# Performance work log

Hardware: AMD Instinct MI355X
Metric: run time of the kernel (lower is better)

Reference implementation:

```python
import jax, jax.numpy as jnp
import numpy as np

B, L, C, H = 4, 2048, 1024, 16
D = C // H  # head_dim = 64


def setup_inputs() -> dict:
    key = jax.random.key(0)
    ks = jax.random.split(key, 7)
    x = jax.random.normal(ks[0], (B, L, C), dtype=jnp.float32)
    Wqkv = jax.random.normal(ks[1], (C, 3 * C), dtype=jnp.float32) * 0.02
    bqkv = jnp.zeros((3 * C,), dtype=jnp.float32)
    q_gamma = jnp.ones((H, D), dtype=jnp.float32)
    k_gamma = jnp.ones((H, D), dtype=jnp.float32)
    Wout = jax.random.normal(ks[2], (C, C), dtype=jnp.float32) * 0.02
    bout = jnp.zeros((C,), dtype=jnp.float32)
    return {"x": x, "Wqkv": Wqkv, "bqkv": bqkv, "q_gamma": q_gamma,
            "k_gamma": k_gamma, "Wout": Wout, "bout": bout}


def _mh_rms_norm(t, gamma):
    # F.normalize(x.float(), dim=-1) * gamma * sqrt(dim), cast back to input dtype
    tf = t.astype(jnp.float32)
    n = jnp.sqrt(jnp.sum(tf * tf, axis=-1, keepdims=True))
    normed = tf / jnp.maximum(n, 1e-12)
    return (normed * gamma * jnp.sqrt(jnp.float32(t.shape[-1]))).astype(t.dtype)


def reference(x, Wqkv, bqkv, q_gamma, k_gamma, Wout, bout):
    b, l, c = x.shape
    qkv = (x @ Wqkv + bqkv).reshape(b, l, 3, H, D)
    q, k, v = qkv[:, :, 0], qkv[:, :, 1], qkv[:, :, 2]  # [B, L, H, D]
    q = _mh_rms_norm(q, q_gamma)
    k = _mh_rms_norm(k, k_gamma)
    # scaled dot-product attention in BLHD layout
    scale = 1.0 / jnp.sqrt(jnp.float32(D))
    scores = jnp.einsum('blhd,bmhd->bhlm', q, k) * scale  # [B, H, L, L]
    probs = jax.nn.softmax(scores, axis=-1)
    h = jnp.einsum('bhlm,bmhd->blhd', probs, v)  # [B, L, H, D]
    h = h.reshape(b, l, c)
    return h @ Wout + bout
```

## Files before the change

kernel.cpp:

```cpp
#include <hip/hip_runtime.h>
#include <hip/hip_bf16.h>
#include <cstdint>
#include <cstddef>

#define B_ 4
#define L_ 2048
#define C_ 1024
#define H_ 16
#define D_ 64

typedef __bf16    bf16x2 __attribute__((ext_vector_type(2)));
typedef __bf16    bf16x4 __attribute__((ext_vector_type(4)));
typedef __bf16    bf16x8 __attribute__((ext_vector_type(8)));
typedef _Float16  f16x4  __attribute__((ext_vector_type(4)));
typedef _Float16  f16x8  __attribute__((ext_vector_type(8)));
typedef float     f32x4  __attribute__((ext_vector_type(4)));

typedef const __attribute__((address_space(1))) uint32_t* gas_ptr;
typedef __attribute__((address_space(3))) uint32_t* las_ptr;
__device__ __forceinline__ void gl_lds16(const void* g, void* l) {
    __builtin_amdgcn_global_load_lds((gas_ptr)(uintptr_t)g,
                                     (las_ptr)(uintptr_t)l, 16, 0, 0);
}

__global__ __launch_bounds__(256) void prep_kernel(
    const float* __restrict__ x, _Float16* __restrict__ x16,
    const float* __restrict__ Wqkv, _Float16* __restrict__ Wq16,
    const float* __restrict__ Wout, _Float16* __restrict__ Wo16)
{
    __shared__ float tile[64][65];
    int bid = blockIdx.x;
    const int tid = threadIdx.x;

    if (bid < 8192) {
        int i = (bid * 256 + tid) * 4;
        float4 v = *(const float4*)&x[i];
        f16x4 o = {(_Float16)v.x, (_Float16)v.y, (_Float16)v.z, (_Float16)v.w};
        *(f16x4*)&x16[i] = o;
        return;
    }
    bid -= 8192;
    const float* W; _Float16* Wt; int N, tx, ty;
    if (bid < 768) { W = Wqkv; Wt = Wq16; N = 3072; tx = bid % 48; ty = bid / 48; }
    else { bid -= 768; W = Wout; Wt = Wo16; N = 1024; tx = bid % 16; ty = bid / 16; }
    const int K = 1024;
    const int k0 = ty * 64, n0 = tx * 64;
    for (int i = tid; i < 1024; i += 256) {
        int r = i >> 4, c4 = (i & 15) * 4;
        float4 v = *(const float4*)&W[(size_t)(k0 + r) * N + n0 + c4];
        tile[r][c4 + 0] = v.x; tile[r][c4 + 1] = v.y;
        tile[r][c4 + 2] = v.z; tile[r][c4 + 3] = v.w;
    }
    __syncthreads();
    for (int i = tid; i < 1024; i += 256) {
        int n = i >> 4, k4 = (i & 15) * 4;
        f16x4 o = {(_Float16)tile[k4 + 0][n], (_Float16)tile[k4 + 1][n],
                   (_Float16)tile[k4 + 2][n], (_Float16)tile[k4 + 3][n]};
        *(f16x4*)&Wt[(size_t)(n0 + n) * K + k0 + k4] = o;
    }
}

template <int MODE>
__global__ __launch_bounds__(256) void gemm_f16_bt_kernel(
    const _Float16* __restrict__ A, const _Float16* __restrict__ Bt,
    const float* __restrict__ bias, void* __restrict__ Cout,
    __bf16* __restrict__ vTout, const float* __restrict__ q_gamma,
    const float* __restrict__ k_gamma, int M, int N, int K)
{
    __shared__ __align__(16) char smraw[MODE == 1 ? 34816 : 16384];
    _Float16* Ash = (_Float16*)smraw;
    _Float16* Bsh = Ash + 128 * 32;

    const int tid  = threadIdx.x;
    const int lane = tid & 63;
    const int wv   = tid >> 6;
    const int wm   = wv & 1, wn = wv >> 1;
    const int n16  = lane & 15, quad = lane >> 4;
    const int brow = blockIdx.y * 128;
    const int bcol = blockIdx.x * 128;

    const int srow = lane >> 2;
    const int scol = (lane & 3) * 8;
    const _Float16* gA = A  + (size_t)(brow + wv * 32 + srow) * K + scol;
    const _Float16* gB = Bt + (size_t)(bcol + wv * 32 + srow) * K + scol;
    _Float16* lA0 = &Ash[wv * 1024];
    _Float16* lA1 = &Ash[wv * 1024 + 512];
    _Float16* lB0 = &Bsh[wv * 1024];
    _Float16* lB1 = &Bsh[wv * 1024 + 512];

    f32x4 acc[4][4] = {};

    for (int k0 = 0; k0 < K; k0 += 32) {
        gl_lds16(gA + k0,                  lA0);
        gl_lds16(gA + k0 + 16 * (size_t)K, lA1);
        gl_lds16(gB + k0,                  lB0);
        gl_lds16(gB + k0 + 16 * (size_t)K, lB1);
        __syncthreads();

        f16x8 ar[4], br[4];
        #pragma unroll
        for (int t = 0; t < 4; t++) {
            ar[t] = *(const f16x8*)&Ash[(wm * 64 + t * 16 + n16) * 32 + quad * 8];
            br[t] = *(const f16x8*)&Bsh[(wn * 64 + t * 16 + n16) * 32 + quad * 8];
        }
        #pragma unroll
        for (int i = 0; i < 4; i++)
            #pragma unroll
            for (int j = 0; j < 4; j++)
                acc[i][j] = __builtin_amdgcn_mfma_f32_16x16x32_f16(
                    ar[i], br[j], acc[i][j], 0, 0, 0);
        __syncthreads();
    }

    if (MODE == 0) {
        #pragma unroll
        for (int j = 0; j < 4; j++) {
            const int col = bcol + wn * 64 + j * 16 + n16;
            const float bv = bias[col];
            #pragma unroll
            for (int i = 0; i < 4; i++) {
                const int row0 = brow + wm * 64 + i * 16 + quad * 4;
                #pragma unroll
                for (int r = 0; r < 4; r++)
                    ((float*)Cout)[(size_t)(row0 + r) * N + col] = acc[i][j][r] + bv;
            }
        }
        return;
    }

    const int region = bcol >> 10;
    float bj[4];
    #pragma unroll
    for (int j = 0; j < 4; j++) bj[j] = bias[bcol + wn * 64 + j * 16 + n16];

    if (region < 2) {
        const float* gamma = (region == 0) ? q_gamma : k_gamma;
        const float scl = (region == 0) ? 1.44269504f : 8.0f;
        const int cb = (bcol & 1023) + wn * 64 + n16;
        float gj[4];
        #pragma unroll
        for (int j = 0; j < 4; j++) gj[j] = gamma[cb + j * 16];

        #pragma unroll
        for (int i = 0; i < 4; i++) {
            #pragma unroll
            for (int r = 0; r < 4; r++) {
                float v0 = acc[i][0][r] + bj[0];
                float v1 = acc[i][1][r] + bj[1];
                float v2 = acc[i][2][r] + bj[2];
                float v3 = acc[i][3][r] + bj[3];
                float ss = v0 * v0 + v1 * v1 + v2 * v2 + v3 * v3;
                ss += __shfl_xor(ss, 1, 64);
                ss += __shfl_xor(ss, 2, 64);
                ss += __shfl_xor(ss, 4, 64);
                ss += __shfl_xor(ss, 8, 64);
                const float sc = scl / fmaxf(sqrtf(ss), 1e-12f);
                const int row = brow + wm * 64 + i * 16 + quad * 4 + r;
                __bf16* op = (__bf16*)Cout + (size_t)row * 3072 + bcol + wn * 64 + n16;
                op[ 0] = (__bf16)(v0 * gj[0] * sc);
                op[16] = (__bf16)(v1 * gj[1] * sc);
                op[32] = (__bf16)(v2 * gj[2] * sc);
                op[48] = (__bf16)(v3 * gj[3] * sc);
            }
        }
    } else {
        __syncthreads();
        __bf16* LT = (__bf16*)smraw;
        #pragma unroll
        for (int i = 0; i < 4; i++)
            #pragma unroll
            for (int j = 0; j < 4; j++) {
                const int col = wn * 64 + j * 16 + n16;
                const int row0 = wm * 64 + i * 16 + quad * 4;
                bf16x4 t4 = {(__bf16)(acc[i][j][0] + bj[j]),
                             (__bf16)(acc[i][j][1] + bj[j]),
                             (__bf16)(acc[i][j][2] + bj[j]),
                             (__bf16)(acc[i][j][3] + bj[j])};
                *(bf16x4*)&LT[col * 136 + row0] = t4;
            }
        __syncthreads();
        const int d = tid >> 1, hf = tid & 1;
        const int bidx = brow >> 11;
        const int l0 = (brow & 2047) + hf * 64;
        const int head = ((bcol - 2048) >> 6) + (d >> 6);
        const size_t vb = (((size_t)(bidx * 16 + head)) * 64 + (d & 63)) * 2048 + l0;
        #pragma unroll
        for (int u = 0; u < 8; u++)
            *(bf16x8*)&vTout[vb + u * 8] = *(const bf16x8*)&LT[d * 136 + hf * 64 + u * 8];
    }
}

__global__ __launch_bounds__(256) void attn_mfma_kernel(
    const __bf16* __restrict__ qkv, const __bf16* __restrict__ vT,
    _Float16* __restrict__ h16)
{
    const int tid  = threadIdx.x;
    const int lane = tid & 63;
    const int wv   = tid >> 6;
    const int n16  = lane & 15;
    const int quad = lane >> 4;
    const int qt = blockIdx.x & 15;
    const int hh = (blockIdx.x >> 4) & 15;
    const int bb = blockIdx.x >> 8;
    const int q0 = qt * 128;
    const int w32 = wv * 32;
    const int bh = bb * 16 + hh;

    __shared__ __align__(16) __bf16 smem[128 * 72 + 4 * 64 * 64];
    __bf16* QP   = smem;
    __bf16* Kbuf = smem + 128 * 72;
    __bf16* Vbuf = Kbuf + 2 * 64 * 64;

    const __bf16* kbase = &qkv[(size_t)(bb * L_) * 3072 + 1024 + hh * 64];
    const __bf16* vbase = &vT[(size_t)bh * 64 * 2048];

    const int lr = lane >> 3;
    const int lc = (lane & 7) ^ lr;
    const __bf16* kpre = kbase + (size_t)(wv * 8 + lr) * 3072 + lc * 8;
    const __bf16* vpre = vbase + (size_t)(wv * 8 + lr) * 2048 + lc * 8;
    __bf16* kdst = Kbuf + (wv * 8) * 64;
    __bf16* vdst = Vbuf + (wv * 8) * 64;

    #pragma unroll
    for (int t = 0; t < 2; t++) {
        gl_lds16(kpre + (size_t)t * 32 * 3072, kdst + t * 2048);
        gl_lds16(vpre + (size_t)t * 32 * 2048, vdst + t * 2048);
    }

    #pragma unroll
    for (int t = 0; t < 4; t++) {
        int i = tid + t * 256;
        int r = i >> 3, d8 = (i & 7) * 8;
        *(bf16x8*)&QP[r * 72 + d8] =
            *(const bf16x8*)&qkv[(size_t)(bb * L_ + q0 + r) * 3072 + hh * 64 + d8];
    }
    __syncthreads();

    bf16x8 qf[2][2];
    #pragma unroll
    for (int qg = 0; qg < 2; qg++)
        #pragma unroll
        for (int hf = 0; hf < 2; hf++)
            qf[qg][hf] = *(const bf16x8*)&QP[(w32 + qg * 16 + n16) * 72 + hf * 32 + quad * 8];
    __syncthreads();

    f32x4 O[2][4] = {};
    float l_run[2] = {0.f, 0.f};

    const int bk0 = n16 * 64 + ((quad)     ^ (n16 & 7)) * 8;
    const int bk1 = n16 * 64 + ((quad + 4) ^ (n16 & 7)) * 8;

    for (int j0 = 0, cur = 0; j0 < L_; j0 += 64, cur ^= 1) {
        if (j0 + 64 < L_) {
            const __bf16* kp = kpre + (size_t)(j0 + 64) * 3072;
            const __bf16* vp = vpre + (j0 + 64);
            __bf16* kd = kdst + (cur ^ 1) * 4096;
            __bf16* vd = vdst + (cur ^ 1) * 4096;
            #pragma unroll
            for (int t = 0; t < 2; t++) {
                gl_lds16(kp + (size_t)t * 32 * 3072, kd + t * 2048);
                gl_lds16(vp + (size_t)t * 32 * 2048, vd + t * 2048);
            }
        }
        const __bf16* Kc = Kbuf + cur * 4096;
        const __bf16* Vc = Vbuf + cur * 4096;

        f32x4 St[2][4] = {};
        __builtin_amdgcn_s_setprio(1);
        #pragma unroll
        for (int kg = 0; kg < 4; kg++) {
            bf16x8 a0 = *(const bf16x8*)&Kc[kg * 1024 + bk0];
            bf16x8 a1 = *(const bf16x8*)&Kc[kg * 1024 + bk1];
            St[0][kg] = __builtin_amdgcn_mfma_f32_16x16x32_bf16(a0, qf[0][0], St[0][kg], 0, 0, 0);
            St[0][kg] = __builtin_amdgcn_mfma_f32_16x16x32_bf16(a1, qf[0][1], St[0][kg], 0, 0, 0);
            St[1][kg] = __builtin_amdgcn_mfma_f32_16x16x32_bf16(a0, qf[1][0], St[1][kg], 0, 0, 0);
            St[1][kg] = __builtin_amdgcn_mfma_f32_16x16x32_bf16(a1, qf[1][1], St[1][kg], 0, 0, 0);
        }
        __builtin_amdgcn_s_setprio(0);

        #pragma unroll
        for (int qg = 0; qg < 2; qg++) {
            const int prow = (w32 + qg * 16 + n16) * 72;
            float ts = 0.f;
            #pragma unroll
            for (int kg = 0; kg < 4; kg++) {
                float p0 = __builtin_amdgcn_exp2f(St[qg][kg][0]);
                float p1 = __builtin_amdgcn_exp2f(St[qg][kg][1]);
                float p2 = __builtin_amdgcn_exp2f(St[qg][kg][2]);
                float p3 = __builtin_amdgcn_exp2f(St[qg][kg][3]);
                bf16x4 t4 = {(__bf16)p0, (__bf16)p1, (__bf16)p2, (__bf16)p3};
                *(bf16x4*)&QP[prow + kg * 16 + quad * 4] = t4;
                ts += (p0 + p1) + (p2 + p3);
            }
            ts += __shfl_xor(ts, 16, 64);
            ts += __shfl_xor(ts, 32, 64);
            l_run[qg] += ts;
        }

        bf16x8 pf[2][2];
        #pragma unroll
        for (int qg = 0; qg < 2; qg++)
            #pragma unroll
            for (int kh = 0; kh < 2; kh++)
                pf[qg][kh] = *(const bf16x8*)&QP[(w32 + qg * 16 + n16) * 72 + kh * 32 + quad * 8];

        __builtin_amdgcn_s_setprio(1);
        #pragma unroll
        for (int dg = 0; dg < 4; dg++) {
            bf16x8 v0 = *(const bf16x8*)&Vc[dg * 1024 + bk0];
            bf16x8 v1 = *(const bf16x8*)&Vc[dg * 1024 + bk1];
            O[0][dg] = __builtin_amdgcn_mfma_f32_16x16x32_bf16(v0, pf[0][0], O[0][dg], 0, 0, 0);
            O[0][dg] = __builtin_amdgcn_mfma_f32_16x16x32_bf16(v1, pf[0][1], O[0][dg], 0, 0, 0);
            O[1][dg] = __builtin_amdgcn_mfma_f32_16x16x32_bf16(v0, pf[1][0], O[1][dg], 0, 0, 0);
            O[1][dg] = __builtin_amdgcn_mfma_f32_16x16x32_bf16(v1, pf[1][1], O[1][dg], 0, 0, 0);
        }
        __builtin_amdgcn_s_setprio(0);

        __syncthreads();
    }

    #pragma unroll
    for (int qg = 0; qg < 2; qg++) {
        const float linv = 1.0f / l_run[qg];
        const int q = q0 + w32 + qg * 16 + n16;
        const size_t orow = (size_t)(bb * L_ + q) * 1024 + hh * 64 + quad * 4;
        #pragma unroll
        for (int dg = 0; dg < 4; dg++) {
            f16x4 o = {(_Float16)(O[qg][dg][0] * linv),
                       (_Float16)(O[qg][dg][1] * linv),
                       (_Float16)(O[qg][dg][2] * linv),
                       (_Float16)(O[qg][dg][3] * linv)};
            *(f16x4*)&h16[orow + dg * 16] = o;
        }
    }
}

extern "C" void kernel_launch(void* const* d_in, const int* in_sizes, int n_in,
                              void* d_out, int out_size, void* d_ws, size_t ws_size,
                              hipStream_t stream)
{
    const float* x       = (const float*)d_in[0];
    const float* Wqkv    = (const float*)d_in[1];
    const float* bqkv    = (const float*)d_in[2];
    const float* q_gamma = (const float*)d_in[3];
    const float* k_gamma = (const float*)d_in[4];
    const float* Wout    = (const float*)d_in[5];
    const float* bout    = (const float*)d_in[6];
    float* out = (float*)d_out;

    uint8_t* ws = (uint8_t*)d_ws;
    _Float16* x16   = (_Float16*)(ws);
    _Float16* Wq16  = (_Float16*)(ws + (16ull << 20));
    _Float16* Wo16  = (_Float16*)(ws + (22ull << 20));
    __bf16*   qkv16 = (__bf16*)  (ws + (24ull << 20));
    _Float16* h16   = (_Float16*)(ws + (72ull << 20));
    __bf16*   vT    = (__bf16*)  (ws + (88ull << 20));

    prep_kernel<<<8192 + 768 + 256, 256, 0, stream>>>(x, x16, Wqkv, Wq16, Wout, Wo16);

    gemm_f16_bt_kernel<1><<<dim3(3 * C_ / 128, B_ * L_ / 128), 256, 0, stream>>>(
        x16, Wq16, bqkv, qkv16, vT, q_gamma, k_gamma, B_ * L_, 3 * C_, C_);

    attn_mfma_kernel<<<B_ * H_ * (L_ / 128), 256, 0, stream>>>(qkv16, vT, h16);

    gemm_f16_bt_kernel<0><<<dim3(C_ / 128, B_ * L_ / 128), 256, 0, stream>>>(
        h16, Wo16, bout, out, nullptr, nullptr, nullptr, B_ * L_, C_, C_);
}
```

Measured before the change: 306.6 us.

## Load V fragments directly from global and drop V LDS staging

V tiles are no longer staged through double-buffered LDS. Each wave now reads its V MFMA fragments straight from the transposed V buffer in global memory, issued after the QK^T MFMAs so the latency can hide behind the softmax. Q fragments are also read directly from global instead of through LDS, and launch bounds ask for 4 blocks per CU. The LDS cut is meant to raise occupancy, but every wave in a block now fetches the same V data separately, which leans on L1/L2 and exposes global latency inside the loop.

```diff
diff --git a/kernel.cpp b/kernel.cpp
--- a/kernel.cpp
+++ b/kernel.cpp
@@ -190,7 +190,7 @@
     }
 }
 
-__global__ __launch_bounds__(256) void attn_mfma_kernel(
+__global__ __launch_bounds__(256, 4) void attn_mfma_kernel(
     const __bf16* __restrict__ qkv, const __bf16* __restrict__ vT,
     _Float16* __restrict__ h16)
 {
@@ -206,10 +206,9 @@
     const int w32 = wv * 32;
     const int bh = bb * 16 + hh;
 
-    __shared__ __align__(16) __bf16 smem[128 * 72 + 4 * 64 * 64];
+    __shared__ __align__(16) __bf16 smem[128 * 72 + 2 * 64 * 64];
     __bf16* QP   = smem;
     __bf16* Kbuf = smem + 128 * 72;
-    __bf16* Vbuf = Kbuf + 2 * 64 * 64;
 
     const __bf16* kbase = &qkv[(size_t)(bb * L_) * 3072 + 1024 + hh * 64];
     const __bf16* vbase = &vT[(size_t)bh * 64 * 2048];
@@ -217,53 +216,39 @@
     const int lr = lane >> 3;
     const int lc = (lane & 7) ^ lr;
     const __bf16* kpre = kbase + (size_t)(wv * 8 + lr) * 3072 + lc * 8;
-    const __bf16* vpre = vbase + (size_t)(wv * 8 + lr) * 2048 + lc * 8;
     __bf16* kdst = Kbuf + (wv * 8) * 64;
-    __bf16* vdst = Vbuf + (wv * 8) * 64;
 
     #pragma unroll
-    for (int t = 0; t < 2; t++) {
+    for (int t = 0; t < 2; t++)
         gl_lds16(kpre + (size_t)t * 32 * 3072, kdst + t * 2048);
-        gl_lds16(vpre + (size_t)t * 32 * 2048, vdst + t * 2048);
-    }
-
-    #pragma unroll
-    for (int t = 0; t < 4; t++) {
-        int i = tid + t * 256;
-        int r = i >> 3, d8 = (i & 7) * 8;
-        *(bf16x8*)&QP[r * 72 + d8] =
-            *(const bf16x8*)&qkv[(size_t)(bb * L_ + q0 + r) * 3072 + hh * 64 + d8];
-    }
-    __syncthreads();
 
     bf16x8 qf[2][2];
+    const __bf16* qrow = &qkv[(size_t)(bb * L_ + q0 + w32 + n16) * 3072 + hh * 64 + quad * 8];
     #pragma unroll
     for (int qg = 0; qg < 2; qg++)
         #pragma unroll
         for (int hf = 0; hf < 2; hf++)
-            qf[qg][hf] = *(const bf16x8*)&QP[(w32 + qg * 16 + n16) * 72 + hf * 32 + quad * 8];
-    __syncthreads();
+            qf[qg][hf] = *(const bf16x8*)&qrow[(size_t)qg * 16 * 3072 + hf * 32];
+
+    const __bf16* vrow = vbase + (size_t)n16 * 2048 + quad * 8;
 
     f32x4 O[2][4] = {};
     float l_run[2] = {0.f, 0.f};
 
     const int bk0 = n16 * 64 + ((quad)     ^ (n16 & 7)) * 8;
     const int bk1 = n16 * 64 + ((quad + 4) ^ (n16 & 7)) * 8;
+
+    __syncthreads();
 
     for (int j0 = 0, cur = 0; j0 < L_; j0 += 64, cur ^= 1) {
         if (j0 + 64 < L_) {
             const __bf16* kp = kpre + (size_t)(j0 + 64) * 3072;
-            const __bf16* vp = vpre + (j0 + 64);
             __bf16* kd = kdst + (cur ^ 1) * 4096;
-            __bf16* vd = vdst + (cur ^ 1) * 4096;
-            #pragma unroll
-            for (int t = 0; t < 2; t++) {
+            #pragma unroll
+            for (int t = 0; t < 2; t++)
                 gl_lds16(kp + (size_t)t * 32 * 3072, kd + t * 2048);
-                gl_lds16(vp + (size_t)t * 32 * 2048, vd + t * 2048);
-            }
         }
         const __bf16* Kc = Kbuf + cur * 4096;
-        const __bf16* Vc = Vbuf + cur * 4096;
 
         f32x4 St[2][4] = {};
         __builtin_amdgcn_s_setprio(1);
@@ -277,6 +262,13 @@
             St[1][kg] = __builtin_amdgcn_mfma_f32_16x16x32_bf16(a1, qf[1][1], St[1][kg], 0, 0, 0);
         }
         __builtin_amdgcn_s_setprio(0);
+
+        bf16x8 vf[4][2];
+        #pragma unroll
+        for (int dg = 0; dg < 4; dg++)
+            #pragma unroll
+            for (int kh = 0; kh < 2; kh++)
+                vf[dg][kh] = *(const bf16x8*)&vrow[(size_t)dg * 16 * 2048 + j0 + kh * 32];
 
         #pragma unroll
         for (int qg = 0; qg < 2; qg++) {
@@ -307,12 +299,10 @@
         __builtin_amdgcn_s_setprio(1);
         #pragma unroll
         for (int dg = 0; dg < 4; dg++) {
-            bf16x8 v0 = *(const bf16x8*)&Vc[dg * 1024 + bk0];
-            bf16x8 v1 = *(const bf16x8*)&Vc[dg * 1024 + bk1];
-            O[0][dg] = __builtin_amdgcn_mfma_f32_16x16x32_bf16(v0, pf[0][0], O[0][dg], 0, 0, 0);
-            O[0][dg] = __builtin_amdgcn_mfma_f32_16x16x32_bf16(v1, pf[0][1], O[0][dg], 0, 0, 0);
-            O[1][dg] = __builtin_amdgcn_mfma_f32_16x16x32_bf16(v0, pf[1][0], O[1][dg], 0, 0, 0);
-            O[1][dg] = __builtin_amdgcn_mfma_f32_16x16x32_bf16(v1, pf[1][1], O[1][dg], 0, 0, 0);
+            O[0][dg] = __builtin_amdgcn_mfma_f32_16x16x32_bf16(vf[dg][0], pf[0][0], O[0][dg], 0, 0, 0);
+            O[0][dg] = __builtin_amdgcn_mfma_f32_16x16x32_bf16(vf[dg][1], pf[0][1], O[0][dg], 0, 0, 0);
+            O[1][dg] = __builtin_amdgcn_mfma_f32_16x16x32_bf16(vf[dg][0], pf[1][0], O[1][dg], 0, 0, 0);
+            O[1][dg] = __builtin_amdgcn_mfma_f32_16x16x32_bf16(vf[dg][1], pf[1][1], O[1][dg], 0, 0, 0);
         }
         __builtin_amdgcn_s_setprio(0);
 
```

Measured after the change: 365.4 us. 19.2% more time.

## Use 32x32x16 MFMA in attention and keep P in registers via permlane swap

Applied to the files above, without the earlier changes.

Rewrites the attention inner loop to use 32x32x16 bf16 MFMA tiles with 32 query rows per wave. The softmax probabilities now go straight from the S accumulator layout into the B-operand layout of the PV MFMA using v_cvt_pk_bf16_f32 and v_permlane32_swap. This removes the LDS round trip for P and the staging of Q through shared memory. LDS use drops, and launch bounds request 4 blocks per SM for occupancy, at the cost of larger register accumulators and reliance on gfx950-specific instructions and layout correctness.

```diff
diff --git a/kernel.cpp b/kernel.cpp
--- a/kernel.cpp
+++ b/kernel.cpp
@@ -15,12 +15,23 @@
 typedef _Float16  f16x4  __attribute__((ext_vector_type(4)));
 typedef _Float16  f16x8  __attribute__((ext_vector_type(8)));
 typedef float     f32x4  __attribute__((ext_vector_type(4)));
+typedef float     f32x16 __attribute__((ext_vector_type(16)));
+typedef uint32_t  u32x4  __attribute__((ext_vector_type(4)));
 
 typedef const __attribute__((address_space(1))) uint32_t* gas_ptr;
 typedef __attribute__((address_space(3))) uint32_t* las_ptr;
 __device__ __forceinline__ void gl_lds16(const void* g, void* l) {
     __builtin_amdgcn_global_load_lds((gas_ptr)(uintptr_t)g,
                                      (las_ptr)(uintptr_t)l, 16, 0, 0);
+}
+
+__device__ __forceinline__ uint32_t cvtpk_bf16(float lo, float hi) {
+    uint32_t r;
+    asm("v_cvt_pk_bf16_f32 %0, %1, %2" : "=v"(r) : "v"(lo), "v"(hi));
+    return r;
+}
+__device__ __forceinline__ void plswap(uint32_t& a, uint32_t& b) {
+    asm("v_permlane32_swap_b32 %0, %1" : "+v"(a), "+v"(b));
 }
 
 __global__ __launch_bounds__(256) void prep_kernel(
@@ -190,26 +201,25 @@
     }
 }
 
-__global__ __launch_bounds__(256) void attn_mfma_kernel(
+__global__ __launch_bounds__(256, 4) void attn_mfma_kernel(
     const __bf16* __restrict__ qkv, const __bf16* __restrict__ vT,
     _Float16* __restrict__ h16)
 {
     const int tid  = threadIdx.x;
     const int lane = tid & 63;
     const int wv   = tid >> 6;
-    const int n16  = lane & 15;
-    const int quad = lane >> 4;
+    const int l31  = lane & 31;
+    const int h    = lane >> 5;
+    const int x7   = l31 & 7;
     const int qt = blockIdx.x & 15;
     const int hh = (blockIdx.x >> 4) & 15;
     const int bb = blockIdx.x >> 8;
     const int q0 = qt * 128;
-    const int w32 = wv * 32;
     const int bh = bb * 16 + hh;
 
-    __shared__ __align__(16) __bf16 smem[128 * 72 + 4 * 64 * 64];
-    __bf16* QP   = smem;
-    __bf16* Kbuf = smem + 128 * 72;
-    __bf16* Vbuf = Kbuf + 2 * 64 * 64;
+    __shared__ __align__(16) __bf16 smem[4 * 4096];
+    __bf16* Kbuf = smem;
+    __bf16* Vbuf = smem + 2 * 4096;
 
     const __bf16* kbase = &qkv[(size_t)(bb * L_) * 3072 + 1024 + hh * 64];
     const __bf16* vbase = &vT[(size_t)bh * 64 * 2048];
@@ -227,111 +237,97 @@
         gl_lds16(vpre + (size_t)t * 32 * 2048, vdst + t * 2048);
     }
 
+    bf16x8 qf[4];
+    const __bf16* qptr = &qkv[(size_t)(bb * L_ + q0 + wv * 32 + l31) * 3072
+                              + hh * 64 + h * 8];
     #pragma unroll
-    for (int t = 0; t < 4; t++) {
-        int i = tid + t * 256;
-        int r = i >> 3, d8 = (i & 7) * 8;
-        *(bf16x8*)&QP[r * 72 + d8] =
-            *(const bf16x8*)&qkv[(size_t)(bb * L_ + q0 + r) * 3072 + hh * 64 + d8];
-    }
+    for (int dk = 0; dk < 4; dk++)
+        qf[dk] = *(const bf16x8*)&qptr[dk * 16];
+
+    f32x16 acc0 = {}, acc1 = {};
+    float l_run = 0.f;
+
     __syncthreads();
-
-    bf16x8 qf[2][2];
-    #pragma unroll
-    for (int qg = 0; qg < 2; qg++)
-        #pragma unroll
-        for (int hf = 0; hf < 2; hf++)
-            qf[qg][hf] = *(const bf16x8*)&QP[(w32 + qg * 16 + n16) * 72 + hf * 32 + quad * 8];
-    __syncthreads();
-
-    f32x4 O[2][4] = {};
-    float l_run[2] = {0.f, 0.f};
-
-    const int bk0 = n16 * 64 + ((quad)     ^ (n16 & 7)) * 8;
-    const int bk1 = n16 * 64 + ((quad + 4) ^ (n16 & 7)) * 8;
 
     for (int j0 = 0, cur = 0; j0 < L_; j0 += 64, cur ^= 1) {
         if (j0 + 64 < L_) {
-            const __bf16* kp = kpre + (size_t)(j0 + 64) * 3072;
-            const __bf16* vp = vpre + (j0 + 64);
-            __bf16* kd = kdst + (cur ^ 1) * 4096;
-            __bf16* vd = vdst + (cur ^ 1) * 4096;
             #pragma unroll
             for (int t = 0; t < 2; t++) {
-                gl_lds16(kp + (size_t)t * 32 * 3072, kd + t * 2048);
-                gl_lds16(vp + (size_t)t * 32 * 2048, vd + t * 2048);
+                gl_lds16(kpre + (size_t)(j0 + 64 + t * 32) * 3072,
+                         kdst + (cur ^ 1) * 4096 + t * 2048);
+                gl_lds16(vpre + (j0 + 64) + (size_t)t * 32 * 2048,
+                         vdst + (cur ^ 1) * 4096 + t * 2048);
             }
         }
         const __bf16* Kc = Kbuf + cur * 4096;
         const __bf16* Vc = Vbuf + cur * 4096;
 
-        f32x4 St[2][4] = {};
+        f32x16 St0 = {}, St1 = {};
         __builtin_amdgcn_s_setprio(1);
         #pragma unroll
-        for (int kg = 0; kg < 4; kg++) {
-            bf16x8 a0 = *(const bf16x8*)&Kc[kg * 1024 + bk0];
-            bf16x8 a1 = *(const bf16x8*)&Kc[kg * 1024 + bk1];
-            St[0][kg] = __builtin_amdgcn_mfma_f32_16x16x32_bf16(a0, qf[0][0], St[0][kg], 0, 0, 0);
-            St[0][kg] = __builtin_amdgcn_mfma_f32_16x16x32_bf16(a1, qf[0][1], St[0][kg], 0, 0, 0);
-            St[1][kg] = __builtin_amdgcn_mfma_f32_16x16x32_bf16(a0, qf[1][0], St[1][kg], 0, 0, 0);
-            St[1][kg] = __builtin_amdgcn_mfma_f32_16x16x32_bf16(a1, qf[1][1], St[1][kg], 0, 0, 0);
+        for (int dk = 0; dk < 4; dk++) {
+            const int co = ((2 * dk + h) ^ x7) * 8;
+            bf16x8 k0 = *(const bf16x8*)&Kc[l31 * 64 + co];
+            bf16x8 k1 = *(const bf16x8*)&Kc[(32 + l31) * 64 + co];
+            St0 = __builtin_amdgcn_mfma_f32_32x32x16_bf16(k0, qf[dk], St0, 0, 0, 0);
+            St1 = __builtin_amdgcn_mfma_f32_32x32x16_bf16(k1, qf[dk], St1, 0, 0, 0);
         }
         __builtin_amdgcn_s_setprio(0);
 
-        #pragma unroll
-        for (int qg = 0; qg < 2; qg++) {
-            const int prow = (w32 + qg * 16 + n16) * 72;
-            float ts = 0.f;
-            #pragma unroll
-            for (int kg = 0; kg < 4; kg++) {
-                float p0 = __builtin_amdgcn_exp2f(St[qg][kg][0]);
-                float p1 = __builtin_amdgcn_exp2f(St[qg][kg][1]);
-                float p2 = __builtin_amdgcn_exp2f(St[qg][kg][2]);
-                float p3 = __builtin_amdgcn_exp2f(St[qg][kg][3]);
-                bf16x4 t4 = {(__bf16)p0, (__bf16)p1, (__bf16)p2, (__bf16)p3};
-                *(bf16x4*)&QP[prow + kg * 16 + quad * 4] = t4;
-                ts += (p0 + p1) + (p2 + p3);
-            }
-            ts += __shfl_xor(ts, 16, 64);
-            ts += __shfl_xor(ts, 32, 64);
-            l_run[qg] += ts;
-        }
-
-        bf16x8 pf[2][2];
-        #pragma unroll
-        for (int qg = 0; qg < 2; qg++)
-            #pragma unroll
-            for (int kh = 0; kh < 2; kh++)
-                pf[qg][kh] = *(const bf16x8*)&QP[(w32 + qg * 16 + n16) * 72 + kh * 32 + quad * 8];
+        bf16x8 pf[4];
+        float ts = 0.f;
+        #pragma unroll
+        for (int th = 0; th < 2; th++) {
+            float e[16];
+            #pragma unroll
+            for (int r = 0; r < 16; r++) {
+                e[r] = __builtin_amdgcn_exp2f(th == 0 ? St0[r] : St1[r]);
+                ts += e[r];
+            }
+            uint32_t a0 = cvtpk_bf16(e[0], e[1]),  a1 = cvtpk_bf16(e[2], e[3]);
+            uint32_t b0 = cvtpk_bf16(e[4], e[5]),  b1 = cvtpk_bf16(e[6], e[7]);
+            plswap(a0, b0); plswap(a1, b1);
+            u32x4 w0; w0.x = a0; w0.y = a1; w0.z = b0; w0.w = b1;
+            pf[th * 2 + 0] = __builtin_bit_cast(bf16x8, w0);
+            uint32_t c0 = cvtpk_bf16(e[8], e[9]),   c1 = cvtpk_bf16(e[10], e[11]);
+            uint32_t d0 = cvtpk_bf16(e[12], e[13]), d1 = cvtpk_bf16(e[14], e[15]);
+            plswap(c0, d0); plswap(c1, d1);
+            u32x4 w1; w1.x = c0; w1.y = c1; w1.z = d0; w1.w = d1;
+            pf[th * 2 + 1] = __builtin_bit_cast(bf16x8, w1);
+        }
+        l_run += ts;
 
         __builtin_amdgcn_s_setprio(1);
         #pragma unroll
-        for (int dg = 0; dg < 4; dg++) {
-            bf16x8 v0 = *(const bf16x8*)&Vc[dg * 1024 + bk0];
-            bf16x8 v1 = *(const bf16x8*)&Vc[dg * 1024 + bk1];
-            O[0][dg] = __builtin_amdgcn_mfma_f32_16x16x32_bf16(v0, pf[0][0], O[0][dg], 0, 0, 0);
-            O[0][dg] = __builtin_amdgcn_mfma_f32_16x16x32_bf16(v1, pf[0][1], O[0][dg], 0, 0, 0);
-            O[1][dg] = __builtin_amdgcn_mfma_f32_16x16x32_bf16(v0, pf[1][0], O[1][dg], 0, 0, 0);
-            O[1][dg] = __builtin_amdgcn_mfma_f32_16x16x32_bf16(v1, pf[1][1], O[1][dg], 0, 0, 0);
+        for (int kq = 0; kq < 4; kq++) {
+            const int co = ((2 * kq + h) ^ x7) * 8;
+            bf16x8 v0 = *(const bf16x8*)&Vc[l31 * 64 + co];
+            bf16x8 v1 = *(const bf16x8*)&Vc[(32 + l31) * 64 + co];
+            acc0 = __builtin_amdgcn_mfma_f32_32x32x16_bf16(v0, pf[kq], acc0, 0, 0, 0);
+            acc1 = __builtin_amdgcn_mfma_f32_32x32x16_bf16(v1, pf[kq], acc1, 0, 0, 0);
         }
         __builtin_amdgcn_s_setprio(0);
 
         __syncthreads();
     }
 
+    l_run += __shfl_xor(l_run, 32, 64);
+    const float linv = 1.0f / l_run;
+
+    const size_t orow = (size_t)(bb * L_ + q0 + wv * 32 + l31) * 1024
+                        + hh * 64 + h * 4;
     #pragma unroll
-    for (int qg = 0; qg < 2; qg++) {
-        const float linv = 1.0f / l_run[qg];
-        const int q = q0 + w32 + qg * 16 + n16;
-        const size_t orow = (size_t)(bb * L_ + q) * 1024 + hh * 64 + quad * 4;
-        #pragma unroll
-        for (int dg = 0; dg < 4; dg++) {
-            f16x4 o = {(_Float16)(O[qg][dg][0] * linv),
-                       (_Float16)(O[qg][dg][1] * linv),
-                       (_Float16)(O[qg][dg][2] * linv),
-                       (_Float16)(O[qg][dg][3] * linv)};
-            *(f16x4*)&h16[orow + dg * 16] = o;
-        }
+    for (int m = 0; m < 4; m++) {
+        f16x4 o0 = {(_Float16)(acc0[4 * m + 0] * linv),
+                    (_Float16)(acc0[4 * m + 1] * linv),
+                    (_Float16)(acc0[4 * m + 2] * linv),
+                    (_Float16)(acc0[4 * m + 3] * linv)};
+        *(f16x4*)&h16[orow + 8 * m] = o0;
+        f16x4 o1 = {(_Float16)(acc1[4 * m + 0] * linv),
+                    (_Float16)(acc1[4 * m + 1] * linv),
+                    (_Float16)(acc1[4 * m + 2] * linv),
+                    (_Float16)(acc1[4 * m + 3] * linv)};
+        *(f16x4*)&h16[orow + 32 + 8 * m] = o1;
     }
 }
 
```

Measured after the change: 298.0 us. 1.03x faster.
